# Kernel optimization log

Hardware: AMD Instinct MI355X
Metric: run time of the kernel (lower is better)

Reference implementation:

```python
import math
import jax
import jax.numpy as jnp
import numpy as np
from jax import lax

B, IC, OC, K, STYLE_DIM, H, W = 16, 512, 512, 3, 512, 32, 32
EPS = 1e-8


def _blur_kernel():
    # make_kernel([1,3,3,1]) outer product, normalized, times upsample_factor**2 (=4)
    k = jnp.array([1.0, 3.0, 3.0, 1.0], dtype=jnp.float32)
    k2 = k[None, :] * k[:, None]
    k2 = k2 / k2.sum()
    return k2 * 4.0  # [4,4]


def setup_inputs() -> dict:
    key = jax.random.key(0)
    k1, k2, k3, k4 = jax.random.split(key, 4)
    return {
        "input": jax.random.normal(k1, (B, IC, H, W), dtype=jnp.float32),
        "style": jax.random.normal(k2, (B, STYLE_DIM), dtype=jnp.float32),
        "weight": jax.random.normal(k3, (1, OC, IC, K, K), dtype=jnp.float32),
        "mod_weight": jax.random.normal(k4, (IC, STYLE_DIM), dtype=jnp.float32),
        "mod_bias": jnp.ones((IC,), dtype=jnp.float32),  # bias_init=1
    }


def reference(input, style, weight, mod_weight, mod_bias):
    batch, in_ch, h, w_sp = input.shape
    out_ch, ksz = weight.shape[1], weight.shape[3]

    # EqualLinear modulation: scale = 1/sqrt(style_dim), lr_mul=1, no activation
    mod_scale = 1.0 / math.sqrt(mod_weight.shape[1])
    s = style @ (mod_weight * mod_scale).T + mod_bias  # [B, IC]

    # modulate + demodulate
    conv_scale = 1.0 / math.sqrt(in_ch * ksz * ksz)
    wmod = conv_scale * weight * s[:, None, :, None, None]  # [B, OC, IC, K, K]
    demod = lax.rsqrt(jnp.sum(wmod * wmod, axis=(2, 3, 4)) + EPS)  # [B, OC]
    wmod = wmod * demod[:, :, None, None, None]

    # conv_transpose2d(stride=2, padding=0, groups=batch) == per-sample conv with
    # lhs_dilation=2, full padding (K-1), spatially flipped kernel in OIHW layout.
    w_conv = wmod[:, :, :, ::-1, ::-1]  # [B, OC, IC, K, K]

    def one_sample(x, wk):
        # x: [IC, H, W], wk: [OC, IC, K, K] -> [OC, 2H+K-2+1, ...] (65x65 here)
        return lax.conv_general_dilated(
            x[None], wk, window_strides=(1, 1),
            padding=[(ksz - 1, ksz - 1)] * 2,
            lhs_dilation=(2, 2),
            dimension_numbers=("NCHW", "OIHW", "NCHW"))[0]

    out = jax.vmap(one_sample)(input, w_conv)  # [B, OC, 65, 65]

    # Blur: upfirdn2d(up=1, down=1, pad=(1,1)) with symmetric 4x4 kernel -> depthwise conv
    bk = _blur_kernel()
    out = jnp.pad(out, ((0, 0), (0, 0), (1, 1), (1, 1)))
    dk = jnp.tile(bk[None, None], (out_ch, 1, 1, 1))  # [OC, 1, 4, 4]
    out = lax.conv_general_dilated(
        out, dk, window_strides=(1, 1), padding="VALID",
        feature_group_count=out_ch,
        dimension_numbers=("NCHW", "OIHW", "NCHW"))  # [B, OC, 64, 64]
    return out
```

## Files before the change

kernel.cpp:

```cpp
#include <hip/hip_runtime.h>
#include <stdint.h>

typedef unsigned int uint32;
typedef unsigned short u16;
typedef short short8 __attribute__((ext_vector_type(8)));
typedef float floatx4 __attribute__((ext_vector_type(4)));

#define OFF_S      0u
#define OFF_DS     32768u
#define OFF_WSUM   65536u
#define OFF_WPACK  1114112u
#define OFF_XST    5832704u
#define OFF_U      22609920u

__device__ __forceinline__ u16 f2bf(float x){
    uint32 u = __float_as_uint(x);
    uint32 r = (u + 0x7FFFu + ((u>>16)&1u)) >> 16;
    return (u16)r;
}
__device__ __forceinline__ float bf2f(u16 h){
    return __uint_as_float(((uint32)h)<<16);
}

#define GLL16(gp, lp) \
    __builtin_amdgcn_global_load_lds( \
        (const __attribute__((address_space(1))) void*)(gp), \
        (__attribute__((address_space(3))) void*)(lp), 16, 0, 0)

__global__ __launch_bounds__(256) void k_style(const float* __restrict__ style,
                                               const float* __restrict__ mw,
                                               const float* __restrict__ mb,
                                               float* __restrict__ s){
    int gid = blockIdx.x*4 + (threadIdx.x>>6);
    int lane = threadIdx.x & 63;
    int b = gid>>9, ic = gid & 511;
    const float* sp = style + b*512;
    const float* wp = mw + (size_t)ic*512;
    float acc = 0.f;
    for (int d=lane; d<512; d+=64) acc += sp[d]*wp[d];
    for (int off=32; off; off>>=1) acc += __shfl_down(acc, off, 64);
    if (lane==0) s[b*512+ic] = acc*0.044194173824159216f + mb[ic];
}

__global__ __launch_bounds__(256) void k_wprep(const float* __restrict__ w,
                                               float* __restrict__ wsum,
                                               u16* __restrict__ wp){
    int idx = blockIdx.x*256 + threadIdx.x;
    const float* p = w + (size_t)idx*9;
    float vv[9]; float a = 0.f;
    #pragma unroll
    for (int t=0;t<9;++t){ float v=p[t]; vv[t]=v; a += v*v; }
    wsum[idx] = a;
    #pragma unroll
    for (int t=0;t<9;++t) wp[(size_t)t*262144 + idx] = f2bf(vv[t]);
}

__global__ __launch_bounds__(256) void k_dscale(const float* __restrict__ s,
                                                const float* __restrict__ wsum,
                                                float* __restrict__ ds){
    int gid = blockIdx.x*4 + (threadIdx.x>>6);
    int lane = threadIdx.x & 63;
    int b = gid>>9, oc = gid & 511;
    const float* sp = s + b*512;
    const float* wp = wsum + (size_t)oc*512;
    float acc=0.f;
    for (int d=lane; d<512; d+=64){ float sv = sp[d]; acc += sv*sv*wp[d]; }
    for (int off=32; off; off>>=1) acc += __shfl_down(acc, off, 64);
    if (lane==0){
        const float cs = 0.014731391274719738f;
        ds[b*512+oc] = cs * rsqrtf(cs*cs*acc + 1e-8f);
    }
}

__global__ __launch_bounds__(256) void k_xst(const float* __restrict__ in,
                                             const float* __restrict__ s,
                                             u16* __restrict__ xst){
    int bx = blockIdx.x;
    int b = bx>>5, i = bx&31;
    __shared__ u16 tr[32*520];
    int tid = threadIdx.x;
    int j = tid & 31;
    for (int ic = tid>>5; ic < 512; ic += 8){
        float v = in[((size_t)(b*512+ic)*32 + i)*32 + j] * s[b*512+ic];
        tr[j*520 + ic] = f2bf(v);
    }
    __syncthreads();
    for (int v = tid; v < 2048; v += 256){
        int jj = v>>6, ic8 = (v&63)*8;
        *(uint4*)(xst + (size_t)(b*1024 + i*32 + jj)*512 + ic8) =
            *(const uint4*)(&tr[jj*520 + ic8]);
    }
}

__global__ __launch_bounds__(512, 2) void k_gemm(const u16* __restrict__ A,
                                                 const u16* __restrict__ Bx,
                                                 u16* __restrict__ C,
                                                 int Ncols){
    int cpx = gridDim.x >> 3;
    int bid = blockIdx.x;
    int swz = (bid & 7)*cpx + (bid >> 3);
    int bx = swz / 18;
    int by = swz - bx*18;
    int m0 = by*256, n0 = bx*256;

    int tid = threadIdx.x;
    int lane = tid & 63;
    int w  = tid >> 6;
    int wm = w >> 2, wn = w & 3;
    int np = lane & 15, qq = lane >> 4;

    __shared__ __align__(16) char smem[131072];

    int rp1 = tid >> 3, sl1 = tid & 7;
    int v1 = sl1 ^ (rp1 & 7);
    int r1 = rp1*2 + ((v1 >> 2) & 1);
    int g1 = v1 & 3;
    const u16* srcA1 = A  + (size_t)(m0 + r1)*512 + g1*8;
    const u16* srcA2 = srcA1 + (size_t)128*512;
    const u16* srcB1 = Bx + (size_t)(n0 + r1)*512 + g1*8;
    const u16* srcB2 = srcB1 + (size_t)128*512;
    int offA1 = (tid & ~63)*8;
    int offA2 = offA1 + 4096;

    #define STAGE(T) do{ \
        u16* _b = (u16*)smem + ((T)&3)*16384; \
        GLL16(srcA1 + (size_t)(T)*32, _b + offA1); \
        GLL16(srcA2 + (size_t)(T)*32, _b + offA2); \
        GLL16(srcB1 + (size_t)(T)*32, _b + 8192 + offA1); \
        GLL16(srcB2 + (size_t)(T)*32, _b + 8192 + offA2); \
    }while(0)

    int rpn = np >> 1;
    int slA = ((qq + ((np & 1) << 2)) ^ rpn) << 3;
    int pAoff = (wm*64 + rpn)*64 + slA;
    int pBoff = (wn*32 + rpn)*64 + slA;

    floatx4 acc[8][4] = {};

    STAGE(0); STAGE(1); STAGE(2);
    asm volatile("s_waitcnt vmcnt(8)" ::: "memory");
    __builtin_amdgcn_s_barrier();

    #pragma unroll
    for (int t = 0; t < 16; ++t){
        if (t < 13) STAGE(t+3);

        const u16* base = (const u16*)smem + (t & 3)*16384;
        short8 af[8], bfr[4];
        #pragma unroll
        for (int mf = 0; mf < 8; ++mf)
            af[mf] = *(const short8*)(base + pAoff + mf*512);
        #pragma unroll
        for (int nf = 0; nf < 4; ++nf)
            bfr[nf] = *(const short8*)(base + 8192 + pBoff + nf*512);

        __builtin_amdgcn_s_setprio(1);
        #pragma unroll
        for (int mf = 0; mf < 8; ++mf)
            #pragma unroll
            for (int nf = 0; nf < 4; ++nf)
                acc[mf][nf] = __builtin_amdgcn_mfma_f32_16x16x32_bf16(
                    af[mf], bfr[nf], acc[mf][nf], 0,0,0);
        __builtin_amdgcn_s_setprio(0);

        if      (t < 13)  asm volatile("s_waitcnt vmcnt(8)" ::: "memory");
        else if (t == 13) asm volatile("s_waitcnt vmcnt(4)" ::: "memory");
        else if (t == 14) asm volatile("s_waitcnt vmcnt(0)" ::: "memory");
        __builtin_amdgcn_s_barrier();
    }
    #undef STAGE

    uint32* Csm32 = (uint32*)smem;
    #pragma unroll
    for (int mf = 0; mf < 8; ++mf){
        #pragma unroll
        for (int nf = 0; nf < 4; ++nf){
            int col = wn*64 + nf*16 + np;
            #pragma unroll
            for (int h = 0; h < 2; ++h){
                int rp = wm*64 + mf*8 + qq*2 + h;
                uint32 v = (uint32)f2bf(acc[mf][nf][2*h]) |
                           ((uint32)f2bf(acc[mf][nf][2*h+1]) << 16);
                Csm32[rp*256 + ((col + rp*8) & 255)] = v;
            }
        }
    }
    __syncthreads();
    #pragma unroll
    for (int i = 0; i < 16; ++i){
        int c = tid + i*512;
        int rp = c >> 6;
        int pc = (c & 63) * 4;
        uint4 v = *(const uint4*)(&Csm32[rp*256 + pc]);
        int lcol = (pc - rp*8) & 255;
        u16* dst = C + (size_t)(m0 + rp*2)*Ncols + n0 + lcol;
        uint2 e, o;
        e.x = (v.x & 0xffffu) | (v.y << 16);
        e.y = (v.z & 0xffffu) | (v.w << 16);
        o.x = (v.x >> 16)     | (v.y & 0xffff0000u);
        o.y = (v.z >> 16)     | (v.w & 0xffff0000u);
        *(uint2*)(dst) = e;
        *(uint2*)(dst + Ncols) = o;
    }
}

__global__ __launch_bounds__(256) void k_blur2(const u16* __restrict__ U,
                                               const float* __restrict__ ds,
                                               float* __restrict__ out,
                                               int b0, int Ncols){
    int oc = blockIdx.x;
    int bp = blockIdx.y;
    int b  = b0 + bp;
    __shared__ __align__(16) u16 Usm[9*1024];
    __shared__ __align__(16) u16 HRsm[3*32*64];
    int tid = threadIdx.x;

    const u16* src0 = U + (size_t)oc*Ncols + (size_t)bp*1024;
    size_t tapstride = (size_t)512 * Ncols;
    #pragma unroll
    for (int it = 0; it < 5; ++it){
        int i = tid + it*256;
        if (i < 1152){
            int tap = i>>7, c8 = i & 127;
            *(uint4*)(&Usm[tap*1024 + c8*8]) =
                *(const uint4*)(src0 + tap*tapstride + c8*8);
        }
    }
    __syncthreads();

    #pragma unroll
    for (int it = 0; it < 12; ++it){
        int task = tid + it*256;
        int a = task >> 10, rem = task & 1023;
        int i = rem >> 5, u = rem & 31;
        const u16* base = Usm + a*3072 + i*32;
        float u0  = bf2f(base[u]);
        float u1  = bf2f(base[1024 + u]);
        float u2  = bf2f(base[2048 + u]);
        float u0p = (u < 31) ? bf2f(base[u + 1])        : 0.f;
        float u1m = (u > 0)  ? bf2f(base[1024 + u - 1]) : 0.f;
        float u1p = (u < 31) ? bf2f(base[1024 + u + 1]) : 0.f;
        float u2m = (u > 0)  ? bf2f(base[2048 + u - 1]) : 0.f;
        float HRe = u1m + 3.f*(u0 + u2m + u1) + u0p + u2;
        float HRo = u0 + u2m + 3.f*(u1 + u0p + u2) + u1p;
        uint32 packed = (uint32)f2bf(HRe) | ((uint32)f2bf(HRo) << 16);
        *(uint32*)(&HRsm[(a*32 + i)*64 + 2*u]) = packed;
    }
    __syncthreads();

    float dsc = ds[b*512 + oc] * (1.f/16.f);
    float* op = out + (size_t)(b*512 + oc) * 4096;
    #pragma unroll
    for (int it = 0; it < 4; ++it){
        int task = tid + it*256;
        int Y = task >> 4, X0 = (task & 15) * 4;
        float o0=0.f,o1=0.f,o2=0.f,o3=0.f;
        int v = Y >> 1;
        #define ACCROW(aa, ii, ww) do{ \
            int _i = (ii); \
            if ((unsigned)_i < 32u){ \
                uint2 rv = *(const uint2*)(&HRsm[((aa)*32 + _i)*64 + X0]); \
                o0 += (ww)*__uint_as_float((rv.x & 0xffffu) << 16); \
                o1 += (ww)*__uint_as_float(rv.x & 0xffff0000u); \
                o2 += (ww)*__uint_as_float((rv.y & 0xffffu) << 16); \
                o3 += (ww)*__uint_as_float(rv.y & 0xffff0000u); \
            } }while(0)
        if ((Y & 1) == 0){
            ACCROW(1, v-1, 1.f);
            ACCROW(0, v,   3.f);
            ACCROW(2, v-1, 3.f);
            ACCROW(1, v,   3.f);
            ACCROW(0, v+1, 1.f);
            ACCROW(2, v,   1.f);
        } else {
            ACCROW(0, v,   1.f);
            ACCROW(2, v-1, 1.f);
            ACCROW(1, v,   3.f);
            ACCROW(0, v+1, 3.f);
            ACCROW(2, v,   3.f);
            ACCROW(1, v+1, 1.f);
        }
        #undef ACCROW
        float4 res = make_float4(dsc*o0, dsc*o1, dsc*o2, dsc*o3);
        *(float4*)(op + Y*64 + X0) = res;
    }
}

extern "C" void kernel_launch(void* const* d_in, const int* in_sizes, int n_in,
                              void* d_out, int out_size, void* d_ws, size_t ws_size,
                              hipStream_t stream){
    const float* input  = (const float*)d_in[0];
    const float* style  = (const float*)d_in[1];
    const float* weight = (const float*)d_in[2];
    const float* mw     = (const float*)d_in[3];
    const float* mb     = (const float*)d_in[4];
    float* out = (float*)d_out;
    char* ws = (char*)d_ws;
    float* s     = (float*)(ws + OFF_S);
    float* ds    = (float*)(ws + OFF_DS);
    float* wsum  = (float*)(ws + OFF_WSUM);
    u16*   wpack = (u16*)(ws + OFF_WPACK);
    u16*   xst   = (u16*)(ws + OFF_XST);
    u16*   U     = (u16*)(ws + OFF_U);

    int NB;
    if      (ws_size >= (size_t)OFF_U + (size_t)4608*16384*2) NB = 16;
    else if (ws_size >= (size_t)OFF_U + (size_t)4608*8192*2)  NB = 8;
    else                                                       NB = 4;
    int npass = 16 / NB;
    int Ncols = NB * 1024;
    int nTilesN = Ncols / 256;

    k_style <<<2048, 256, 0, stream>>>(style, mw, mb, s);
    k_wprep <<<1024, 256, 0, stream>>>(weight, wsum, wpack);
    k_dscale<<<2048, 256, 0, stream>>>(s, wsum, ds);
    k_xst   <<<512,  256, 0, stream>>>(input, s, xst);

    for (int p = 0; p < npass; ++p){
        const u16* xp = xst + (size_t)p * NB * 1024 * 512;
        k_gemm <<<dim3(18*nTilesN), 512, 0, stream>>>(wpack, xp, U, Ncols);
        k_blur2<<<dim3(512, NB),       256, 0, stream>>>(U, ds, out, p*NB, Ncols);
    }
}
```

Baseline: 339.4 us.

## Split GEMM k-step into two phases interleaving LDS reads, global prefetch and MFMA

Each k-iteration of the bf16 MFMA GEMM loop now runs in two halves. The first half loads four A fragments plus the B fragments and issues the A-tile prefetch, then computes. The second half loads the remaining A fragments and issues the B-tile prefetch, then computes. Extra barriers and lgkmcnt waits are added to keep waves in lockstep, in a ping-pong style schedule. The aim is to overlap LDS reads and global loads with MFMA work and to reduce register pressure, at the cost of more barriers per iteration.

```diff
diff --git a/kernel.cpp b/kernel.cpp
--- a/kernel.cpp
+++ b/kernel.cpp
@@ -122,14 +122,6 @@
     int offA1 = (tid & ~63)*8;
     int offA2 = offA1 + 4096;
 
-    #define STAGE(T) do{ \
-        u16* _b = (u16*)smem + ((T)&3)*16384; \
-        GLL16(srcA1 + (size_t)(T)*32, _b + offA1); \
-        GLL16(srcA2 + (size_t)(T)*32, _b + offA2); \
-        GLL16(srcB1 + (size_t)(T)*32, _b + 8192 + offA1); \
-        GLL16(srcB2 + (size_t)(T)*32, _b + 8192 + offA2); \
-    }while(0)
-
     int rpn = np >> 1;
     int slA = ((qq + ((np & 1) << 2)) ^ rpn) << 3;
     int pAoff = (wm*64 + rpn)*64 + slA;
@@ -137,38 +129,71 @@
 
     floatx4 acc[8][4] = {};
 
-    STAGE(0); STAGE(1); STAGE(2);
+    #define STAGE_A(T) do{ \
+        u16* _b = (u16*)smem + ((T)&3)*16384; \
+        GLL16(srcA1 + (size_t)(T)*32, _b + offA1); \
+        GLL16(srcA2 + (size_t)(T)*32, _b + offA2); \
+    }while(0)
+    #define STAGE_B(T) do{ \
+        u16* _b = (u16*)smem + ((T)&3)*16384; \
+        GLL16(srcB1 + (size_t)(T)*32, _b + 8192 + offA1); \
+        GLL16(srcB2 + (size_t)(T)*32, _b + 8192 + offA2); \
+    }while(0)
+
+    STAGE_A(0); STAGE_B(0);
+    STAGE_A(1); STAGE_B(1);
+    STAGE_A(2); STAGE_B(2);
     asm volatile("s_waitcnt vmcnt(8)" ::: "memory");
     __builtin_amdgcn_s_barrier();
 
     #pragma unroll
     for (int t = 0; t < 16; ++t){
-        if (t < 13) STAGE(t+3);
-
         const u16* base = (const u16*)smem + (t & 3)*16384;
-        short8 af[8], bfr[4];
-        #pragma unroll
-        for (int mf = 0; mf < 8; ++mf)
+        short8 af[4], bfr[4];
+
+        #pragma unroll
+        for (int mf = 0; mf < 4; ++mf)
             af[mf] = *(const short8*)(base + pAoff + mf*512);
         #pragma unroll
         for (int nf = 0; nf < 4; ++nf)
             bfr[nf] = *(const short8*)(base + 8192 + pBoff + nf*512);
-
+        if (t < 13) STAGE_A(t+3);
+
+        __builtin_amdgcn_s_barrier();
+        asm volatile("s_waitcnt lgkmcnt(0)" ::: "memory");
         __builtin_amdgcn_s_setprio(1);
         #pragma unroll
-        for (int mf = 0; mf < 8; ++mf)
+        for (int mf = 0; mf < 4; ++mf)
             #pragma unroll
             for (int nf = 0; nf < 4; ++nf)
                 acc[mf][nf] = __builtin_amdgcn_mfma_f32_16x16x32_bf16(
                     af[mf], bfr[nf], acc[mf][nf], 0,0,0);
         __builtin_amdgcn_s_setprio(0);
+        __builtin_amdgcn_s_barrier();
+
+        #pragma unroll
+        for (int mf = 0; mf < 4; ++mf)
+            af[mf] = *(const short8*)(base + pAoff + (mf+4)*512);
+        if (t < 13) STAGE_B(t+3);
+
+        __builtin_amdgcn_s_barrier();
+        asm volatile("s_waitcnt lgkmcnt(0)" ::: "memory");
+        __builtin_amdgcn_s_setprio(1);
+        #pragma unroll
+        for (int mf = 0; mf < 4; ++mf)
+            #pragma unroll
+            for (int nf = 0; nf < 4; ++nf)
+                acc[mf+4][nf] = __builtin_amdgcn_mfma_f32_16x16x32_bf16(
+                    af[mf], bfr[nf], acc[mf+4][nf], 0,0,0);
+        __builtin_amdgcn_s_setprio(0);
 
         if      (t < 13)  asm volatile("s_waitcnt vmcnt(8)" ::: "memory");
         else if (t == 13) asm volatile("s_waitcnt vmcnt(4)" ::: "memory");
         else if (t == 14) asm volatile("s_waitcnt vmcnt(0)" ::: "memory");
         __builtin_amdgcn_s_barrier();
     }
-    #undef STAGE
+    #undef STAGE_A
+    #undef STAGE_B
 
     uint32* Csm32 = (uint32*)smem;
     #pragma unroll
```

Result: no change. 340.6 us (+0.4%).

## Double-buffer GEMM LDS fragments in registers to overlap reads with MFMA

Applied to the files above, without the earlier changes.

The bf16 MFMA main loop now keeps two sets of A/B fragment registers. While the MFMAs for tile T run on one set, the fragments for tile T+1 are loaded from LDS into the other set, so LDS read latency is hidden behind matrix math. The loop is restructured into a barrier-first body with adjusted vmcnt waits, and a final __syncthreads is added before the epilogue reuses shared memory. This costs roughly 48 more VGPRs per thread for the second fragment set, which could lower occupancy or cause spills.

```diff
diff --git a/kernel.cpp b/kernel.cpp
--- a/kernel.cpp
+++ b/kernel.cpp
@@ -2,6 +2,7 @@
 #include <stdint.h>
 
 typedef unsigned int uint32;
+typedef unsigned long long u64;
 typedef unsigned short u16;
 typedef short short8 __attribute__((ext_vector_type(8)));
 typedef float floatx4 __attribute__((ext_vector_type(4)));
@@ -122,14 +123,6 @@
     int offA1 = (tid & ~63)*8;
     int offA2 = offA1 + 4096;
 
-    #define STAGE(T) do{ \
-        u16* _b = (u16*)smem + ((T)&3)*16384; \
-        GLL16(srcA1 + (size_t)(T)*32, _b + offA1); \
-        GLL16(srcA2 + (size_t)(T)*32, _b + offA2); \
-        GLL16(srcB1 + (size_t)(T)*32, _b + 8192 + offA1); \
-        GLL16(srcB2 + (size_t)(T)*32, _b + 8192 + offA2); \
-    }while(0)
-
     int rpn = np >> 1;
     int slA = ((qq + ((np & 1) << 2)) ^ rpn) << 3;
     int pAoff = (wm*64 + rpn)*64 + slA;
@@ -137,38 +130,72 @@
 
     floatx4 acc[8][4] = {};
 
-    STAGE(0); STAGE(1); STAGE(2);
-    asm volatile("s_waitcnt vmcnt(8)" ::: "memory");
+    #define STAGE_A(T) do{ \
+        u16* _b = (u16*)smem + ((T)&3)*16384; \
+        GLL16(srcA1 + (size_t)(T)*32, _b + offA1); \
+        GLL16(srcA2 + (size_t)(T)*32, _b + offA2); \
+    }while(0)
+    #define STAGE_B(T) do{ \
+        u16* _b = (u16*)smem + ((T)&3)*16384; \
+        GLL16(srcB1 + (size_t)(T)*32, _b + 8192 + offA1); \
+        GLL16(srcB2 + (size_t)(T)*32, _b + 8192 + offA2); \
+    }while(0)
+    #define CFENCE asm volatile("" ::: "memory")
+
+    short8 af0[8], bf0[4], af1[8], bf1[4];
+
+    STAGE_A(0); STAGE_B(0);
+    STAGE_A(1); STAGE_B(1);
+    STAGE_A(2); STAGE_B(2);
+    asm volatile("s_waitcnt vmcnt(4)" ::: "memory");
     __builtin_amdgcn_s_barrier();
-
-    #pragma unroll
-    for (int t = 0; t < 16; ++t){
-        if (t < 13) STAGE(t+3);
-
-        const u16* base = (const u16*)smem + (t & 3)*16384;
-        short8 af[8], bfr[4];
+    CFENCE;
+    {
+        const u16* b0 = (const u16*)smem;
         #pragma unroll
         for (int mf = 0; mf < 8; ++mf)
-            af[mf] = *(const short8*)(base + pAoff + mf*512);
+            af0[mf] = *(const short8*)(b0 + pAoff + mf*512);
         #pragma unroll
         for (int nf = 0; nf < 4; ++nf)
-            bfr[nf] = *(const short8*)(base + 8192 + pBoff + nf*512);
-
-        __builtin_amdgcn_s_setprio(1);
-        #pragma unroll
-        for (int mf = 0; mf < 8; ++mf)
-            #pragma unroll
-            for (int nf = 0; nf < 4; ++nf)
-                acc[mf][nf] = __builtin_amdgcn_mfma_f32_16x16x32_bf16(
-                    af[mf], bfr[nf], acc[mf][nf], 0,0,0);
-        __builtin_amdgcn_s_setprio(0);
-
-        if      (t < 13)  asm volatile("s_waitcnt vmcnt(8)" ::: "memory");
-        else if (t == 13) asm volatile("s_waitcnt vmcnt(4)" ::: "memory");
-        else if (t == 14) asm volatile("s_waitcnt vmcnt(0)" ::: "memory");
-        __builtin_amdgcn_s_barrier();
-    }
-    #undef STAGE
+            bf0[nf] = *(const short8*)(b0 + 8192 + pBoff + nf*512);
+    }
+
+    #define BODY(T, AC, BC, AN, BN) do{ \
+        __builtin_amdgcn_s_barrier(); \
+        CFENCE; \
+        if ((T) < 13){ STAGE_A((T)+3); STAGE_B((T)+3); } \
+        __builtin_amdgcn_s_setprio(1); \
+        if ((T) < 15){ \
+            const u16* nb = (const u16*)smem + (((T)+1)&3)*16384; \
+            _Pragma("unroll") \
+            for (int mf = 0; mf < 8; ++mf) \
+                AN[mf] = *(const short8*)(nb + pAoff + mf*512); \
+            _Pragma("unroll") \
+            for (int nf = 0; nf < 4; ++nf) \
+                BN[nf] = *(const short8*)(nb + 8192 + pBoff + nf*512); \
+        } \
+        _Pragma("unroll") \
+        for (int mf = 0; mf < 8; ++mf) \
+            _Pragma("unroll") \
+            for (int nf = 0; nf < 4; ++nf) \
+                acc[mf][nf] = __builtin_amdgcn_mfma_f32_16x16x32_bf16( \
+                    AC[mf], BC[nf], acc[mf][nf], 0,0,0); \
+        __builtin_amdgcn_s_setprio(0); \
+        if ((T) < 13)       asm volatile("s_waitcnt vmcnt(4)" ::: "memory"); \
+        else if ((T) == 13) asm volatile("s_waitcnt vmcnt(0)" ::: "memory"); \
+    }while(0)
+
+    #pragma unroll
+    for (int tt = 0; tt < 8; ++tt){
+        BODY(2*tt,   af0, bf0, af1, bf1);
+        BODY(2*tt+1, af1, bf1, af0, bf0);
+    }
+    #undef BODY
+    #undef STAGE_A
+    #undef STAGE_B
+    #undef CFENCE
+
+    __syncthreads();
 
     uint32* Csm32 = (uint32*)smem;
     #pragma unroll
```

Result: faster. 332.1 us (-2.1%).

## Shrink GEMM tile to 256x128 with double buffering for higher occupancy

Applied to the files above, without the earlier changes.

The GEMM block tile shrinks from 256x256 to 256x128. LDS use drops from 128KB to 48KB (two stages instead of four), accumulators halve, and launch bounds rise to 4 blocks per CU. The block-to-tile swizzle is rewritten to group rows in threes for L2 reuse, and the epilogue stages output through LDS in two chunks. The aim is more concurrent blocks to hide latency, at the cost of lower arithmetic intensity per block, a shallower prefetch pipeline with a full vmcnt(0) wait every iteration, and more global reads of A.

```diff
diff --git a/kernel.cpp b/kernel.cpp
--- a/kernel.cpp
+++ b/kernel.cpp
@@ -2,6 +2,7 @@
 #include <stdint.h>
 
 typedef unsigned int uint32;
+typedef unsigned long long u64;
 typedef unsigned short u16;
 typedef short short8 __attribute__((ext_vector_type(8)));
 typedef float floatx4 __attribute__((ext_vector_type(4)));
@@ -92,115 +93,127 @@
     }
 }
 
-__global__ __launch_bounds__(512, 2) void k_gemm(const u16* __restrict__ A,
+__global__ __launch_bounds__(512, 4) void k_gemm(const u16* __restrict__ A,
                                                  const u16* __restrict__ Bx,
                                                  u16* __restrict__ C,
                                                  int Ncols){
-    int cpx = gridDim.x >> 3;
-    int bid = blockIdx.x;
-    int swz = (bid & 7)*cpx + (bid >> 3);
-    int bx = swz / 18;
-    int by = swz - bx*18;
-    int m0 = by*256, n0 = bx*256;
+    int x = blockIdx.x & 7;
+    int s = blockIdx.x >> 3;
+    int SBX = (Ncols >> 7) >> 3;
+    int st  = s / (3*SBX);
+    int r   = s - st*(3*SBX);
+    int by  = st*3 + r/SBX;
+    int bx  = x*SBX + (r - (r/SBX)*SBX);
+    int m0 = by*256, n0 = bx*128;
 
     int tid = threadIdx.x;
     int lane = tid & 63;
     int w  = tid >> 6;
-    int wm = w >> 2, wn = w & 3;
+    int wm = w >> 1, wn = w & 1;
     int np = lane & 15, qq = lane >> 4;
 
-    __shared__ __align__(16) char smem[131072];
+    __shared__ __align__(16) char smem[49152];
 
     int rp1 = tid >> 3, sl1 = tid & 7;
     int v1 = sl1 ^ (rp1 & 7);
-    int r1 = rp1*2 + ((v1 >> 2) & 1);
+    int r1 = 2*rp1 + ((v1 >> 2) & 1);
     int g1 = v1 & 3;
     const u16* srcA1 = A  + (size_t)(m0 + r1)*512 + g1*8;
     const u16* srcA2 = srcA1 + (size_t)128*512;
     const u16* srcB1 = Bx + (size_t)(n0 + r1)*512 + g1*8;
-    const u16* srcB2 = srcB1 + (size_t)128*512;
     int offA1 = (tid & ~63)*8;
     int offA2 = offA1 + 4096;
+    int offB  = 8192 + offA1;
+
+    int rpn = np >> 1;
+    int slA = ((qq + ((np & 1) << 2)) ^ rpn) << 3;
+    int pAoff = (wm*32 + rpn)*64 + slA;
+    int pBoff = (wn*32 + rpn)*64 + slA;
+
+    floatx4 acc[4][4] = {};
 
     #define STAGE(T) do{ \
-        u16* _b = (u16*)smem + ((T)&3)*16384; \
+        u16* _b = (u16*)smem + ((T)&1)*12288; \
         GLL16(srcA1 + (size_t)(T)*32, _b + offA1); \
         GLL16(srcA2 + (size_t)(T)*32, _b + offA2); \
-        GLL16(srcB1 + (size_t)(T)*32, _b + 8192 + offA1); \
-        GLL16(srcB2 + (size_t)(T)*32, _b + 8192 + offA2); \
+        GLL16(srcB1 + (size_t)(T)*32, _b + offB); \
     }while(0)
-
-    int rpn = np >> 1;
-    int slA = ((qq + ((np & 1) << 2)) ^ rpn) << 3;
-    int pAoff = (wm*64 + rpn)*64 + slA;
-    int pBoff = (wn*32 + rpn)*64 + slA;
-
-    floatx4 acc[8][4] = {};
-
-    STAGE(0); STAGE(1); STAGE(2);
-    asm volatile("s_waitcnt vmcnt(8)" ::: "memory");
+    #define CFENCE asm volatile("" ::: "memory")
+
+    STAGE(0);
+    asm volatile("s_waitcnt vmcnt(0)" ::: "memory");
     __builtin_amdgcn_s_barrier();
+    CFENCE;
 
     #pragma unroll
     for (int t = 0; t < 16; ++t){
-        if (t < 13) STAGE(t+3);
-
-        const u16* base = (const u16*)smem + (t & 3)*16384;
-        short8 af[8], bfr[4];
+        const u16* base = (const u16*)smem + (t & 1)*12288;
+        short8 af[4], bfr[4];
         #pragma unroll
-        for (int mf = 0; mf < 8; ++mf)
+        for (int mf = 0; mf < 4; ++mf)
             af[mf] = *(const short8*)(base + pAoff + mf*512);
         #pragma unroll
         for (int nf = 0; nf < 4; ++nf)
             bfr[nf] = *(const short8*)(base + 8192 + pBoff + nf*512);
+        if (t < 15) STAGE(t+1);
 
         __builtin_amdgcn_s_setprio(1);
         #pragma unroll
-        for (int mf = 0; mf < 8; ++mf)
+        for (int mf = 0; mf < 4; ++mf)
             #pragma unroll
             for (int nf = 0; nf < 4; ++nf)
                 acc[mf][nf] = __builtin_amdgcn_mfma_f32_16x16x32_bf16(
                     af[mf], bfr[nf], acc[mf][nf], 0,0,0);
         __builtin_amdgcn_s_setprio(0);
 
-        if      (t < 13)  asm volatile("s_waitcnt vmcnt(8)" ::: "memory");
-        else if (t == 13) asm volatile("s_waitcnt vmcnt(4)" ::: "memory");
-        else if (t == 14) asm volatile("s_waitcnt vmcnt(0)" ::: "memory");
-        __builtin_amdgcn_s_barrier();
+        if (t < 15){
+            asm volatile("s_waitcnt vmcnt(0)" ::: "memory");
+            __builtin_amdgcn_s_barrier();
+            CFENCE;
+        }
     }
     #undef STAGE
+    #undef CFENCE
+
+    __syncthreads();
 
     uint32* Csm32 = (uint32*)smem;
     #pragma unroll
-    for (int mf = 0; mf < 8; ++mf){
+    for (int ch = 0; ch < 2; ++ch){
+        if ((wm >> 1) == ch){
+            #pragma unroll
+            for (int mf = 0; mf < 4; ++mf){
+                #pragma unroll
+                for (int nf = 0; nf < 4; ++nf){
+                    int col = wn*64 + nf*16 + np;
+                    #pragma unroll
+                    for (int h = 0; h < 2; ++h){
+                        int rp = (wm&1)*32 + mf*8 + qq*2 + h;
+                        uint32 v = (uint32)f2bf(acc[mf][nf][2*h]) |
+                                   ((uint32)f2bf(acc[mf][nf][2*h+1]) << 16);
+                        Csm32[rp*128 + ((col + rp*8) & 127)] = v;
+                    }
+                }
+            }
+        }
+        __syncthreads();
         #pragma unroll
-        for (int nf = 0; nf < 4; ++nf){
-            int col = wn*64 + nf*16 + np;
-            #pragma unroll
-            for (int h = 0; h < 2; ++h){
-                int rp = wm*64 + mf*8 + qq*2 + h;
-                uint32 v = (uint32)f2bf(acc[mf][nf][2*h]) |
-                           ((uint32)f2bf(acc[mf][nf][2*h+1]) << 16);
-                Csm32[rp*256 + ((col + rp*8) & 255)] = v;
-            }
-        }
-    }
-    __syncthreads();
-    #pragma unroll
-    for (int i = 0; i < 16; ++i){
-        int c = tid + i*512;
-        int rp = c >> 6;
-        int pc = (c & 63) * 4;
-        uint4 v = *(const uint4*)(&Csm32[rp*256 + pc]);
-        int lcol = (pc - rp*8) & 255;
-        u16* dst = C + (size_t)(m0 + rp*2)*Ncols + n0 + lcol;
-        uint2 e, o;
-        e.x = (v.x & 0xffffu) | (v.y << 16);
-        e.y = (v.z & 0xffffu) | (v.w << 16);
-        o.x = (v.x >> 16)     | (v.y & 0xffff0000u);
-        o.y = (v.z >> 16)     | (v.w & 0xffff0000u);
-        *(uint2*)(dst) = e;
-        *(uint2*)(dst + Ncols) = o;
+        for (int i = 0; i < 4; ++i){
+            int c = tid + i*512;
+            int rp = c >> 5;
+            int pc = (c & 31) * 4;
+            uint4 v = *(const uint4*)(&Csm32[rp*128 + pc]);
+            int lcol = (pc - rp*8) & 127;
+            u16* dst = C + (size_t)(m0 + ch*128 + rp*2)*Ncols + n0 + lcol;
+            uint2 e, o;
+            e.x = (v.x & 0xffffu) | (v.y << 16);
+            e.y = (v.z & 0xffffu) | (v.w << 16);
+            o.x = (v.x >> 16)     | (v.y & 0xffff0000u);
+            o.y = (v.z >> 16)     | (v.w & 0xffff0000u);
+            *(uint2*)(dst) = e;
+            *(uint2*)(dst + Ncols) = o;
+        }
+        __syncthreads();
     }
 }
 
@@ -309,7 +322,6 @@
     else                                                       NB = 4;
     int npass = 16 / NB;
     int Ncols = NB * 1024;
-    int nTilesN = Ncols / 256;
 
     k_style <<<2048, 256, 0, stream>>>(style, mw, mb, s);
     k_wprep <<<1024, 256, 0, stream>>>(weight, wsum, wpack);
@@ -318,7 +330,7 @@
 
     for (int p = 0; p < npass; ++p){
         const u16* xp = xst + (size_t)p * NB * 1024 * 512;
-        k_gemm <<<dim3(18*nTilesN), 512, 0, stream>>>(wpack, xp, U, Ncols);
-        k_blur2<<<dim3(512, NB),       256, 0, stream>>>(U, ds, out, p*NB, Ncols);
-    }
-}
+        k_gemm <<<dim3(18 * (Ncols/128)), 512, 0, stream>>>(wpack, xp, U, Ncols);
+        k_blur2<<<dim3(512, NB),          256, 0, stream>>>(U, ds, out, p*NB, Ncols);
+    }
+}
```

New measurement: 330.1 us. 1.03x faster.
